# Performance work log

Measured on AMD Instinct MI355X. Metric: run time of the kernel, lower is better.

## Reference

```python
import jax, jax.numpy as jnp
import numpy as np


def leaky(x):
    return jnp.where(x > 0, x, 0.2 * x)


def conv(x, w, b, s, p):
    y = jax.lax.conv_general_dilated(x, w, (s, s), [(p, p), (p, p)],
                                     dimension_numbers=('NCHW', 'OIHW', 'NCHW'))
    return y + b[None, :, None, None]


def maxpool2s1(x):
    return jax.lax.reduce_window(x, -jnp.inf, jax.lax.max, (1, 1, 2, 2), (1, 1, 1, 1), 'VALID')


def bn_eval(x, g, b, m, v):
    scale = g / jnp.sqrt(v + 1e-5)
    return (x - m[None, :, None, None]) * scale[None, :, None, None] + b[None, :, None, None]


def adaptive_avg_pool(x, oh, ow):
    # matches torch AdaptiveAvgPool2d window rule: [floor(i*H/o), ceil((i+1)*H/o))
    B, C, H, W = x.shape
    rows = []
    for i in range(oh):
        hs, he = (i * H) // oh, -((-(i + 1) * H) // oh)
        cols = []
        for j in range(ow):
            ws, we = (j * W) // ow, -((-(j + 1) * W) // ow)
            cols.append(x[:, :, hs:he, ws:we].mean((2, 3)))
        rows.append(jnp.stack(cols, -1))
    return jnp.stack(rows, -2)  # [B,C,oh,ow]


def forward(x, tw1, tb1, tw2, tb2, tw3, tb3, tw4, tb4,
            sw1, sb1, bn1_g, bn1_b, bn1_m, bn1_v,
            sw2, sb2, bn2_g, bn2_b, bn2_m, bn2_v,
            cw, cb, ew1, eb1, ew2, eb2, ew3, eb3):
    B = x.shape[0]
    E, K = ew1.shape[0], 2
    # --- scout router (BN in eval mode with running stats) ---
    h = jax.nn.relu(bn_eval(conv(x, sw1, sb1, 4, 3), bn1_g, bn1_b, bn1_m, bn1_v))
    h = jax.nn.relu(bn_eval(conv(h, sw2, sb2, 2, 1), bn2_g, bn2_b, bn2_m, bn2_v))
    logits = h.mean((2, 3)) @ cw.T + cb                       # [B,E]
    gate = jax.nn.softmax(logits, axis=-1)
    topk_p, topk_i = jax.lax.top_k(gate, K)                   # [B,K]
    topk_p = topk_p / (topk_p.sum(-1, keepdims=True) + 1e-6)
    # --- shared trunk ---
    t = maxpool2s1(leaky(conv(x, tw1, tb1, 4, 1)))            # 224->56->55
    t = maxpool2s1(leaky(conv(t, tw2, tb2, 2, 2)))            # 55->28->27
    t = leaky(conv(t, tw3, tb3, 1, 1))                        # 27
    t = maxpool2s1(leaky(conv(t, tw4, tb4, 1, 1)))            # 27->26
    t = adaptive_avg_pool(t, 3, 3)                            # [B,128,3,3]
    flat = t.reshape(B, -1)                                   # [B,1152]
    # --- MoE head: dense per-expert MLP, masked weighted combine ---
    h1 = leaky(jnp.einsum('bi,eoi->beo', flat, ew1) + eb1[None])   # [B,E,1024]
    h2 = leaky(jnp.einsum('beh,eoh->beo', h1, ew2) + eb2[None])    # [B,E,512]
    h3 = jnp.einsum('beh,eoh->beo', h2, ew3) + eb3[None]           # [B,E,feat]
    onehot = (topk_i[:, :, None] == jnp.arange(E)[None, None, :])  # [B,K,E]
    comb_w = jnp.sum(topk_p[:, :, None] * onehot, axis=1)          # [B,E]
    out = jnp.einsum('beo,be->bo', h3, comb_w)                     # [B,feat]
    return out


def setup_inputs() -> dict:
    key = jax.random.key(0)
    ks = jax.random.split(key, 32)
    W = 0.02
    d = {}
    d['x'] = jax.random.normal(ks[0], (256, 3, 224, 224), jnp.float32)
    d['tw1'] = jax.random.normal(ks[1], (16, 3, 3, 3), jnp.float32) * W
    d['tb1'] = jnp.zeros((16,), jnp.float32)
    d['tw2'] = jax.random.normal(ks[2], (32, 16, 5, 5), jnp.float32) * W
    d['tb2'] = jnp.zeros((32,), jnp.float32)
    d['tw3'] = jax.random.normal(ks[3], (64, 32, 3, 3), jnp.float32) * W
    d['tb3'] = jnp.zeros((64,), jnp.float32)
    d['tw4'] = jax.random.normal(ks[4], (128, 64, 3, 3), jnp.float32) * W
    d['tb4'] = jnp.zeros((128,), jnp.float32)
    d['sw1'] = jax.random.normal(ks[5], (16, 3, 7, 7), jnp.float32) * W
    d['sb1'] = jnp.zeros((16,), jnp.float32)
    d['bn1_g'] = jnp.ones((16,), jnp.float32)
    d['bn1_b'] = jnp.zeros((16,), jnp.float32)
    d['bn1_m'] = jnp.zeros((16,), jnp.float32)
    d['bn1_v'] = jnp.ones((16,), jnp.float32)
    d['sw2'] = jax.random.normal(ks[6], (32, 16, 3, 3), jnp.float32) * W
    d['sb2'] = jnp.zeros((32,), jnp.float32)
    d['bn2_g'] = jnp.ones((32,), jnp.float32)
    d['bn2_b'] = jnp.zeros((32,), jnp.float32)
    d['bn2_m'] = jnp.zeros((32,), jnp.float32)
    d['bn2_v'] = jnp.ones((32,), jnp.float32)
    d['cw'] = jax.random.normal(ks[7], (3, 32), jnp.float32) * W
    d['cb'] = jnp.zeros((3,), jnp.float32)
    d['ew1'] = jax.random.normal(ks[8], (3, 1024, 1152), jnp.float32) * W
    d['eb1'] = jnp.zeros((3, 1024), jnp.float32)
    d['ew2'] = jax.random.normal(ks[9], (3, 512, 1024), jnp.float32) * W
    d['eb2'] = jnp.zeros((3, 512), jnp.float32)
    d['ew3'] = jax.random.normal(ks[10], (3, 512, 512), jnp.float32) * W
    d['eb3'] = jnp.zeros((3, 512), jnp.float32)
    return d


def reference(x, tw1, tb1, tw2, tb2, tw3, tb3, tw4, tb4,
              sw1, sb1, bn1_g, bn1_b, bn1_m, bn1_v,
              sw2, sb2, bn2_g, bn2_b, bn2_m, bn2_v,
              cw, cb, ew1, eb1, ew2, eb2, ew3, eb3):
    return forward(x, tw1, tb1, tw2, tb2, tw3, tb3, tw4, tb4,
                   sw1, sb1, bn1_g, bn1_b, bn1_m, bn1_v,
                   sw2, sb2, bn2_g, bn2_b, bn2_m, bn2_v,
                   cw, cb, ew1, eb1, ew2, eb2, ew3, eb3)
```

## Files before the change

### kernel.cpp

```cpp
#include <hip/hip_runtime.h>

#define DEV static __device__ __forceinline__

constexpr int BATCH = 256;

DEV float leakyf(float x){ return x > 0.f ? x : 0.2f * x; }

typedef _Float16 f16x8 __attribute__((ext_vector_type(8)));
typedef float f32x4 __attribute__((ext_vector_type(4)));

DEV f16x8 max8(f16x8 a, f16x8 b){
  f16x8 r;
  #pragma unroll
  for (int j = 0; j < 8; ++j) r[j] = a[j] > b[j] ? a[j] : b[j];
  return r;
}

template<int IC,int OC>
DEV void wpackM_body(int i, const float* __restrict__ w, _Float16* __restrict__ wp){
  constexpr int F = OC/16;
  int j = i & 7, L = (i >> 3) & 63, rest = i >> 9;
  int f = rest % F; int q2 = rest / F; int s = q2 % (IC/32); int t = q2 / (IC/32);
  int oc = f*16 + (L & 15), ic = s*32 + (L >> 4)*8 + j;
  wp[i] = (_Float16)w[((size_t)oc*IC + ic)*9 + t];
}

template<int OC,int K>
DEV void wpackS_body(int i, const float* __restrict__ w, _Float16* __restrict__ wp){
  constexpr int F = OC/16, KWP = (K+1)/2;
  int j = i & 7, L = (i >> 3) & 63, rest = i >> 9;
  int f = rest % F, s = rest / F;
  int kh = s / KWP, kwp = s % KWP;
  int k = (L >> 4)*8 + j;
  int kw = 2*kwp + (k >> 4), ic = k & 15;
  int oc = f*16 + (L & 15);
  float v = (kw < K) ? w[((size_t)(oc*16 + ic)*K + kh)*K + kw] : 0.f;
  wp[i] = (_Float16)v;
}

DEV void wpackF_body(int i, const float* __restrict__ sw1,
                     const float* __restrict__ tw1, _Float16* __restrict__ wp){
  int j = i & 7, L = (i >> 3) & 63, rest = i >> 9;
  int nf = rest & 1, s = rest >> 1;
  int k = s*32 + (L >> 4)*8 + j;
  int oc = L & 15;
  int t = k / 48, c = k % 48;
  int dr = (t >> 1) - 1, dc = (t & 1) - 1;
  int ic = c >> 4, pr = (c >> 2) & 3, pc = c & 3;
  float v = 0.f;
  if (nf == 0){
    int kh = 4*dr + pr + 3, kw = 4*dc + pc + 3;
    if (kh >= 0 && kh < 7 && kw >= 0 && kw < 7) v = sw1[((oc*3 + ic)*7 + kh)*7 + kw];
  } else {
    int kh = 4*dr + pr + 1, kw = 4*dc + pc + 1;
    if (kh >= 0 && kh < 3 && kw >= 0 && kw < 3) v = tw1[((oc*3 + ic)*3 + kh)*3 + kw];
  }
  wp[i] = (_Float16)v;
}

template<int KTOT>
DEV void wpackG_body(int i, int e, const float* __restrict__ w, int N,
                     _Float16* __restrict__ wp){
  const int NF = N >> 4;
  const int total = NF * (KTOT >> 5) * 512;
  w  += (size_t)e * N * KTOT;
  wp += (size_t)e * total;
  int j = i & 7, L = (i >> 3) & 63, rest = i >> 9;
  int nf = rest % NF, t = rest / NF;
  int n = nf*16 + (L & 15), k = t*32 + (L >> 4)*8 + j;
  wp[i] = (_Float16)w[(size_t)n*KTOT + k];
}

__global__ __launch_bounds__(256) void wpackX_k(
    const float* __restrict__ tw3, _Float16* __restrict__ wpk3,
    const float* __restrict__ tw4, _Float16* __restrict__ wpk4,
    const float* __restrict__ tw2, _Float16* __restrict__ wp2,
    const float* __restrict__ sw2, _Float16* __restrict__ wps2,
    const float* __restrict__ sw1, const float* __restrict__ tw1,
    _Float16* __restrict__ wpf,
    const float* __restrict__ ew1, _Float16* __restrict__ ewp1,
    const float* __restrict__ ew2, _Float16* __restrict__ ewp2,
    const float* __restrict__ ew3, _Float16* __restrict__ ewp3){
  const int b = blockIdx.x;
  const int tid = threadIdx.x;
  if (b < 72){
    wpackM_body<32,64>(b*256 + tid, tw3, wpk3);
  } else if (b < 360){
    wpackM_body<64,128>((b-72)*256 + tid, tw4, wpk4);
  } else if (b < 420){
    wpackS_body<32,5>((b-360)*256 + tid, tw2, wp2);
  } else if (b < 444){
    wpackS_body<32,3>((b-420)*256 + tid, sw2, wps2);
  } else if (b < 468){
    wpackF_body((b-444)*256 + tid, sw1, tw1, wpf);
  } else {
    int t = b - 468;
    if (t < 13824){
      wpackG_body<1152>((t % 4608)*256 + tid, t / 4608, ew1, 1024, ewp1);
    } else if (t < 19968){
      int t2 = t - 13824;
      wpackG_body<1024>((t2 % 2048)*256 + tid, t2 / 2048, ew2, 512, ewp2);
    } else {
      int t3 = t - 19968;
      wpackG_body<512>((t3 % 1024)*256 + tid, t3 / 1024, ew3, 512, ewp3);
    }
  }
}

__global__ __launch_bounds__(256) void fusedM_k(
    const float* __restrict__ x,
    const _Float16* __restrict__ W,
    const float* __restrict__ sb, const float* __restrict__ cb_,
    const float* __restrict__ g, const float* __restrict__ bt,
    const float* __restrict__ mn, const float* __restrict__ vr,
    _Float16* __restrict__ s1out, _Float16* __restrict__ c1out){
  __shared__ __align__(16) _Float16 Ah[3*58*64];
  const int tid = threadIdx.x;
  const int n = blockIdx.x / 28, oh0 = (blockIdx.x % 28) * 2;

  if (tid < 48){
    int rr = tid >> 4, side = (tid >> 3) & 1, q = tid & 7;
    int col = side ? 57 : 0;
    *(int4*)((char*)Ah + (((rr*58 + col) << 7) + q*16)) = (int4){0,0,0,0};
  }

  {
    const int m = tid & 63;
    const bool mok = (m < 56);
    const int cc = m + 1;
    int rc0 = tid >> 6;
    int ic   = (rc0 == 3) ? 0 : rc0;
    int ridx = (rc0 == 3) ? 1 : 0;
    #pragma unroll
    for (int j = 0; j < 9; ++j){
      const int ih = 4*oh0 - 4 + ridx;
      if (mok){
        float4 v = {0.f,0.f,0.f,0.f};
        if (ih >= 0)
          v = *(const float4*)(x + ((size_t)(n*3 + ic)*224 + ih)*224 + 4*m);
        const int rr = ridx >> 2, pr = ridx & 3;
        int boff = (((rr*58 + cc) << 7) + ic*32 + pr*8) ^ ((cc & 7) << 4);
        _Float16 h4[4] = {(_Float16)v.x, (_Float16)v.y, (_Float16)v.z, (_Float16)v.w};
        *(unsigned long long*)((char*)Ah + boff) = *(unsigned long long*)h4;
      }
      ic += 1; ridx += 1;
      if (ic >= 3){ ic -= 3; ridx += 1; }
    }
  }
  __syncthreads();

  const int wid = tid >> 6, lane = tid & 63;
  const int kg8 = (lane >> 4) * 8;
  f32x4 acc[2][2];
  #pragma unroll
  for (int mi = 0; mi < 2; ++mi)
    #pragma unroll
    for (int nf = 0; nf < 2; ++nf) acc[mi][nf] = (f32x4){0.f,0.f,0.f,0.f};

  #pragma unroll
  for (int s = 0; s < 6; ++s){
    const int kk = s*32 + kg8;
    const int t = kk / 48, c0 = kk - t*48;
    const int ra = t >> 1, ca = t & 1;
    f16x8 ah[2];
    #pragma unroll
    for (int mi = 0; mi < 2; ++mi){
      const int m = 2*wid + mi;
      const int rowsel = m >> 2;
      const int ow = (m & 3)*16 + (lane & 15);
      const int owc = ow > 55 ? 55 : ow;
      const int col = owc + ca;
      const int bidx = ((((rowsel + ra)*58 + col) << 7) + c0*2) ^ ((col & 7) << 4);
      ah[mi] = *(const f16x8*)((const char*)Ah + bidx);
    }
    #pragma unroll
    for (int nf = 0; nf < 2; ++nf){
      const f16x8 bw = *(const f16x8*)(W + (s*2 + nf)*512 + lane*8);
      #pragma unroll
      for (int mi = 0; mi < 2; ++mi)
        acc[mi][nf] = __builtin_amdgcn_mfma_f32_16x16x32_f16(ah[mi], bw, acc[mi][nf], 0,0,0);
    }
  }

  const int oc = lane & 15;
  const float sbv = sb[oc];
  const float scv = g[oc] * __frsqrt_rn(vr[oc] + 1e-5f);
  const float mnv = mn[oc], btv = bt[oc], cbv = cb_[oc];
  #pragma unroll
  for (int mi = 0; mi < 2; ++mi){
    const int m = 2*wid + mi;
    const int row = oh0 + (m >> 2);
    const int owb = (m & 3)*16 + (lane >> 4)*4;
    #pragma unroll
    for (int r = 0; r < 4; ++r){
      const int ow = owb + r;
      if (ow >= 56) continue;
      float vs = acc[mi][0][r] + sbv;
      vs = fmaxf((vs - mnv)*scv + btv, 0.f);
      const size_t o = (((size_t)n*56 + row)*56 + ow)*16 + oc;
      s1out[o] = (_Float16)vs;
      c1out[o] = (_Float16)leakyf(acc[mi][1][r] + cbv);
    }
  }
}

template<int OC,int K,int P,int IH,int IW,int ACT,bool OUT16,bool GATE,bool POOLIN>
DEV void convS_body(int bx, int tid, _Float16* A, float* gred,
    const _Float16* __restrict__ in,
    const _Float16* __restrict__ W,
    const float* __restrict__ bias,
    const float* __restrict__ bng, const float* __restrict__ bnb,
    const float* __restrict__ bnm, const float* __restrict__ bnv,
    float* __restrict__ outF, _Float16* __restrict__ outH,
    float* __restrict__ gsum){
  constexpr int F = OC/16, KWP = (K+1)/2;
  constexpr int RW = POOLIN ? (IW+1) : IW;

  const int n = bx / 28, oh = bx % 28;

  if (GATE && tid < 32) gred[tid] = 0.f;

  for (int i = tid; i < K*60*2; i += 256){
    int half = i & 1; int p = i >> 1;
    int c = p % 60; int r = p / 60;
    int ih = 2*oh - P + r, iw = c - P;
    int4 v = {0,0,0,0};
    if (ih >= 0 && ih < IH && iw >= 0 && iw < IW){
      const _Float16* q = in + (((size_t)n*(POOLIN ? IH+1 : IH) + ih)*RW + iw)*16 + half*8;
      if (POOLIN){
        f16x8 a = *(const f16x8*)q;
        f16x8 b = *(const f16x8*)(q + 16);
        f16x8 cc = *(const f16x8*)(q + RW*16);
        f16x8 d = *(const f16x8*)(q + RW*16 + 16);
        f16x8 mx = max8(max8(a, b), max8(cc, d));
        v = *(int4*)&mx;
      } else {
        v = *(const int4*)q;
      }
    }
    int byte = ((r*60 + c)*32 + half*16) ^ (((c>>1)&7) << 4);
    *(int4*)((char*)A + byte) = v;
  }
  __syncthreads();

  const int wid = tid >> 6, lane = tid & 63;
  const int fsel = wid & 1, mb = wid >> 1;
  const int ow_l = min(mb*16 + (lane & 15), 27);
  const int ic0b = ((lane >> 4) & 1) * 16;
  const int kwo  = (lane >> 4) >> 1;

  f32x4 acc = {0.f,0.f,0.f,0.f};
  #pragma unroll
  for (int kh = 0; kh < K; ++kh){
    #pragma unroll
    for (int kwp = 0; kwp < KWP; ++kwp){
      const int kw = 2*kwp + kwo;
      const int c = 2*ow_l + kw;
      int byte = ((kh*60 + c)*32 + ic0b) ^ (((c>>1)&7) << 4);
      f16x8 a = *(const f16x8*)((const char*)A + byte);
      const int s = kh*KWP + kwp;
      const f16x8 b = *(const f16x8*)(W + (s*F + fsel)*512 + lane*8);
      acc = __builtin_amdgcn_mfma_f32_16x16x32_f16(a, b, acc, 0,0,0);
    }
  }

  const int oc = fsel*16 + (lane & 15);
  float bv = bias[oc], sc = 1.f, mm = 0.f, bb = 0.f;
  if (ACT == 1){
    sc = bng[oc] * __frsqrt_rn(bnv[oc] + 1e-5f);
    mm = bnm[oc]; bb = bnb[oc];
  }
  float lsum = 0.f;
  #pragma unroll
  for (int r = 0; r < 4; ++r){
    const int ow = mb*16 + (lane >> 4)*4 + r;
    if (ow >= 28) continue;
    float v = acc[r] + bv;
    if (ACT == 1) v = fmaxf((v - mm)*sc + bb, 0.f);
    else          v = leakyf(v);
    if (GATE){
      lsum += v;
    } else {
      const size_t o = (((size_t)n*28 + oh)*28 + ow)*OC + oc;
      if (OUT16) outH[o] = (_Float16)v;
      else       outF[o] = v;
    }
  }
  if (GATE){
    atomicAdd(&gred[oc], lsum);
    __syncthreads();
    if (tid < 32) atomicAdd(&gsum[n*32 + tid], gred[tid]);
  }
}

__global__ __launch_bounds__(256) void convSS_k(
    const _Float16* __restrict__ s1h, const _Float16* __restrict__ wps2,
    const float* __restrict__ sb2,
    const float* __restrict__ bn2g, const float* __restrict__ bn2b,
    const float* __restrict__ bn2m, const float* __restrict__ bn2v,
    float* __restrict__ gsum,
    const _Float16* __restrict__ c1h, const _Float16* __restrict__ wp2,
    const float* __restrict__ tb2, _Float16* __restrict__ c2h){
  __shared__ __align__(16) _Float16 A[5*60*16];
  __shared__ float gred[32];
  const int tid = threadIdx.x;
  if (blockIdx.x < BATCH*28){
    convS_body<32,3,1,56,56,1,false,true,false>(blockIdx.x, tid, A, gred,
        s1h, wps2, sb2, bn2g, bn2b, bn2m, bn2v, nullptr, nullptr, gsum);
  } else {
    convS_body<32,5,2,55,55,0,true,false,true>(blockIdx.x - BATCH*28, tid, A, gred,
        c1h, wp2, tb2, nullptr, nullptr, nullptr, nullptr, nullptr, c2h, nullptr);
  }
}

template<int IC,int OC,bool POOLIN>
__global__ __launch_bounds__(256) void convM_k(
    const _Float16* __restrict__ Ag,
    const _Float16* __restrict__ W,
    const float* __restrict__ bias,
    _Float16* __restrict__ Out)
{
  constexpr int S = IC/32, FTOT = OC/16, FW = FTOT/2;
  constexpr int ICB = IC*2, ICG = ICB/16;
  __shared__ __align__(16) char A[4*34*ICB];

  const int tid = threadIdx.x;
  const int bx = blockIdx.x;
  const int n = bx / 14, pr = bx % 14;
  const int oh0 = pr * 2;

  for (int g = tid; g < 4*34*ICG; g += 256){
    int r = g / (34*ICG);
    int rem = g - r*(34*ICG);
    int c = rem / ICG, q = rem - c*ICG;
    int ir = oh0 + r - 1, icol = c - 1;
    int4 v = {0,0,0,0};
    if (ir >= 0 && ir < 27 && icol >= 0 && icol < 27){
      if (POOLIN){
        const _Float16* p0 = Ag + (((size_t)n*28 + ir)*28 + icol)*IC + q*8;
        f16x8 a = *(const f16x8*)p0;
        f16x8 b = *(const f16x8*)(p0 + IC);
        f16x8 cc = *(const f16x8*)(p0 + 28*IC);
        f16x8 d = *(const f16x8*)(p0 + 28*IC + IC);
        f16x8 mx = max8(max8(a, b), max8(cc, d));
        v = *(int4*)&mx;
      } else {
        v = *(const int4*)(Ag + (((size_t)n*27 + ir)*27 + icol)*IC + q*8);
      }
    }
    int off = (r*34 + c)*ICB + q*16;
    int swz = off ^ ((c & 7) << 4);
    *(int4*)(A + swz) = v;
  }
  __syncthreads();

  const int wid = tid >> 6, lane = tid & 63;
  const int rsel = wid & 1, ocq = wid >> 1;
  const int c0 = lane & 15, kg = (lane >> 4) * 16;
  const int colb0 = c0*ICB + kg, colb1 = (16 + c0)*ICB + kg;
  int msk[3];
  #pragma unroll
  for (int kw = 0; kw < 3; ++kw) msk[kw] = ((c0 + kw) & 7) << 4;

  f32x4 acc[2][FW];
  #pragma unroll
  for (int m = 0; m < 2; ++m)
    #pragma unroll
    for (int f = 0; f < FW; ++f) acc[m][f] = (f32x4){0.f,0.f,0.f,0.f};

  #pragma unroll
  for (int kh = 0; kh < 3; ++kh){
    #pragma unroll
    for (int kw = 0; kw < 3; ++kw){
      #pragma unroll
      for (int s = 0; s < S; ++s){
        const int fr0 = (((kh*3 + kw)*S + s)*FTOT + ocq*FW) * 512 + lane*8;
        f16x8 b[FW];
        #pragma unroll
        for (int f = 0; f < FW; ++f)
          b[f] = *(const f16x8*)(W + fr0 + f*512);
        const int base = ((rsel + kh)*34 + kw)*ICB + s*64;
        const int o0 = (base + colb0) ^ msk[kw];
        const int o1 = (base + colb1) ^ msk[kw];
        f16x8 a0 = *(const f16x8*)(A + o0);
        f16x8 a1 = *(const f16x8*)(A + o1);
        #pragma unroll
        for (int f = 0; f < FW; ++f){
          acc[0][f] = __builtin_amdgcn_mfma_f32_16x16x32_f16(a0, b[f], acc[0][f], 0,0,0);
          acc[1][f] = __builtin_amdgcn_mfma_f32_16x16x32_f16(a1, b[f], acc[1][f], 0,0,0);
        }
      }
    }
  }

  const int orow = oh0 + rsel;
  if (orow >= 27) return;
  #pragma unroll
  for (int f = 0; f < FW; ++f){
    const int oc = (ocq*FW + f)*16 + c0;
    const float bv = bias[oc];
    #pragma unroll
    for (int m = 0; m < 2; ++m){
      #pragma unroll
      for (int r = 0; r < 4; ++r){
        const int ow = m*16 + (lane >> 4)*4 + r;
        if (ow >= 27) continue;
        float v = leakyf(acc[m][f][r] + bv);
        Out[(((size_t)n*27 + orow)*27 + ow)*OC + oc] = (_Float16)v;
      }
    }
  }
}

template<int KTOT,int ACT>
__global__ __launch_bounds__(256) void gemmH_k(
    const _Float16* __restrict__ A, long strideA,
    const _Float16* __restrict__ W,
    const float* __restrict__ bias, int N,
    _Float16* __restrict__ OutH){
  const int e = blockIdx.z;
  A += (size_t)e * strideA;
  const int NF = N >> 4, KT = KTOT >> 5;
  W += (size_t)e * NF * KT * 512;
  const float* bs = bias + (size_t)e * N;
  const size_t ob = (size_t)e * 256 * N;

  const int tid = threadIdx.x, wid = tid >> 6, lane = tid & 63;
  const int mblk = blockIdx.x * 32;
  const int nf = blockIdx.y * 4 + wid;
  const int r0 = mblk + (lane & 15);
  const int kof = (lane >> 4) * 8;

  f32x4 acc0 = {0,0,0,0}, acc1 = {0,0,0,0};
  for (int t = 0; t < KT; ++t){
    const int k = t*32 + kof;
    f16x8 a0 = *(const f16x8*)(A + (size_t)r0*KTOT + k);
    f16x8 a1 = *(const f16x8*)(A + (size_t)(r0+16)*KTOT + k);
    const f16x8 b = *(const f16x8*)(W + ((size_t)t*NF + nf)*512 + lane*8);
    acc0 = __builtin_amdgcn_mfma_f32_16x16x32_f16(a0, b, acc0, 0,0,0);
    acc1 = __builtin_amdgcn_mfma_f32_16x16x32_f16(a1, b, acc1, 0,0,0);
  }
  const int n = nf*16 + (lane & 15);
  const float bv = bs[n];
  #pragma unroll
  for (int mi = 0; mi < 2; ++mi){
    f32x4 a = mi ? acc1 : acc0;
    #pragma unroll
    for (int r = 0; r < 4; ++r){
      const int m = mblk + mi*16 + (lane >> 4)*4 + r;
      float v = a[r] + bv;
      if (ACT == 1) v = leakyf(v);
      OutH[ob + (size_t)m*N + n] = (_Float16)v;
    }
  }
}

__global__ __launch_bounds__(256) void gemmC_k(
    const _Float16* __restrict__ A,
    const _Float16* __restrict__ W,
    const float* __restrict__ b3,
    const float* __restrict__ gsum,
    const float* __restrict__ cw, const float* __restrict__ cb,
    float* __restrict__ out){
  __shared__ float combL[16][3];
  const int tid = threadIdx.x, wid = tid >> 6, lane = tid & 63;
  const int mblk = blockIdx.x * 16;

  if (tid < 16){
    const int n = mblk + tid;
    float mch[32];
    #pragma unroll
    for (int c = 0; c < 32; ++c) mch[c] = gsum[n*32 + c] / 784.f;
    float lg[3];
    #pragma unroll
    for (int e = 0; e < 3; ++e){
      float a = cb[e];
      #pragma unroll
      for (int c = 0; c < 32; ++c) a += mch[c] * cw[e*32 + c];
      lg[e] = a;
    }
    float m = fmaxf(lg[0], fmaxf(lg[1], lg[2]));
    float ex[3], sum = 0.f;
    #pragma unroll
    for (int e = 0; e < 3; ++e){ ex[e] = expf(lg[e] - m); sum += ex[e]; }
    float pr[3];
    #pragma unroll
    for (int e = 0; e < 3; ++e) pr[e] = ex[e] / sum;
    int i1 = 0;
    if (pr[1] > pr[0]) i1 = 1;
    if (pr[2] > pr[i1]) i1 = 2;
    int i2 = -1;
    for (int e = 0; e < 3; ++e){
      if (e == i1) continue;
      if (i2 < 0 || pr[e] > pr[i2]) i2 = e;
    }
    float s12 = pr[i1] + pr[i2] + 1e-6f;
    float cmb[3] = {0.f, 0.f, 0.f};
    cmb[i1] = pr[i1] / s12;
    cmb[i2] = pr[i2] / s12;
    combL[tid][0] = cmb[0];
    combL[tid][1] = cmb[1];
    combL[tid][2] = cmb[2];
  }
  __syncthreads();

  const int nf = blockIdx.y * 4 + wid;
  const int r0 = mblk + (lane & 15);
  const int kof = (lane >> 4) * 8;
  const int n = nf*16 + (lane & 15);

  f32x4 oacc = {0.f,0.f,0.f,0.f};
  #pragma unroll
  for (int e = 0; e < 3; ++e){
    const _Float16* Ae = A + (size_t)e * 256 * 512;
    const _Float16* We = W + (size_t)e * 32 * 16 * 512;
    f32x4 acc = {0.f,0.f,0.f,0.f};
    for (int t = 0; t < 16; ++t){
      f16x8 a = *(const f16x8*)(Ae + (size_t)r0*512 + t*32 + kof);
      const f16x8 b = *(const f16x8*)(We + ((size_t)t*32 + nf)*512 + lane*8);
      acc = __builtin_amdgcn_mfma_f32_16x16x32_f16(a, b, acc, 0,0,0);
    }
    const float bv = b3[e*512 + n];
    #pragma unroll
    for (int r = 0; r < 4; ++r){
      const int lr = (lane >> 4)*4 + r;
      oacc[r] += combL[lr][e] * (acc[r] + bv);
    }
  }
  #pragma unroll
  for (int r = 0; r < 4; ++r){
    const int m = mblk + (lane >> 4)*4 + r;
    out[(size_t)m*512 + n] = oacc[r];
  }
}

__global__ __launch_bounds__(256) void papool2_k(const _Float16* __restrict__ in,
                                                 _Float16* __restrict__ flat16){
  __shared__ float red[2][128][9];
  const int n = blockIdx.x;
  const int tid = threadIdx.x;
  const int h = tid >> 7, c = tid & 127;
  const _Float16* p = in + (size_t)n * 729 * 128 + c;

  float sum[9];
  #pragma unroll
  for (int j = 0; j < 9; ++j) sum[j] = 0.f;

  float prev[27], cur[27];
  const int r0 = h * 13;
  #pragma unroll
  for (int rr = 0; rr < 14; ++rr){
    const int r = r0 + rr;
    #pragma unroll
    for (int cc = 0; cc < 27; ++cc)
      cur[cc] = (float)p[(size_t)(r*27 + cc) * 128];
    if (rr > 0){
      const int pr = r - 1;
      const bool b0 = (pr < 9), b1 = (pr >= 8) && (pr < 18), b2 = (pr >= 17);
      #pragma unroll
      for (int cc = 0; cc < 26; ++cc){
        float v = fmaxf(fmaxf(prev[cc], prev[cc+1]), fmaxf(cur[cc], cur[cc+1]));
        if (b0){
          if (cc < 9)             sum[0] += v;
          if (cc >= 8 && cc < 18) sum[1] += v;
          if (cc >= 17)           sum[2] += v;
        }
        if (b1){
          if (cc < 9)             sum[3] += v;
          if (cc >= 8 && cc < 18) sum[4] += v;
          if (cc >= 17)           sum[5] += v;
        }
        if (b2){
          if (cc < 9)             sum[6] += v;
          if (cc >= 8 && cc < 18) sum[7] += v;
          if (cc >= 17)           sum[8] += v;
        }
      }
    }
    #pragma unroll
    for (int cc = 0; cc < 27; ++cc) prev[cc] = cur[cc];
  }

  #pragma unroll
  for (int j = 0; j < 9; ++j) red[h][c][j] = sum[j];
  __syncthreads();

  if (tid < 128){
    const float rcp[9] = {1.f/81, 1.f/90, 1.f/81, 1.f/90, 1.f/100, 1.f/90,
                          1.f/81, 1.f/90, 1.f/81};
    _Float16* o = flat16 + (size_t)n * 1152 + tid * 9;
    #pragma unroll
    for (int j = 0; j < 9; ++j)
      o[j] = (_Float16)((red[0][tid][j] + red[1][tid][j]) * rcp[j]);
  }
}

extern "C" void kernel_launch(void* const* d_in, const int* in_sizes, int n_in,
                              void* d_out, int out_size, void* d_ws, size_t ws_size,
                              hipStream_t stream){
  const float* x    = (const float*)d_in[0];
  const float* tw1  = (const float*)d_in[1];  const float* tb1 = (const float*)d_in[2];
  const float* tw2  = (const float*)d_in[3];  const float* tb2 = (const float*)d_in[4];
  const float* tw3  = (const float*)d_in[5];  const float* tb3 = (const float*)d_in[6];
  const float* tw4  = (const float*)d_in[7];  const float* tb4 = (const float*)d_in[8];
  const float* sw1  = (const float*)d_in[9];  const float* sb1 = (const float*)d_in[10];
  const float* bn1g = (const float*)d_in[11]; const float* bn1b = (const float*)d_in[12];
  const float* bn1m = (const float*)d_in[13]; const float* bn1v = (const float*)d_in[14];
  const float* sw2  = (const float*)d_in[15]; const float* sb2 = (const float*)d_in[16];
  const float* bn2g = (const float*)d_in[17]; const float* bn2b = (const float*)d_in[18];
  const float* bn2m = (const float*)d_in[19]; const float* bn2v = (const float*)d_in[20];
  const float* cw   = (const float*)d_in[21]; const float* cb  = (const float*)d_in[22];
  const float* ew1  = (const float*)d_in[23]; const float* eb1 = (const float*)d_in[24];
  const float* ew2  = (const float*)d_in[25]; const float* eb2 = (const float*)d_in[26];
  const float* ew3  = (const float*)d_in[27]; const float* eb3 = (const float*)d_in[28];
  float* out = (float*)d_out;

  float* ws = (float*)d_ws;
  size_t off = 0;
  _Float16* flat16 = (_Float16*)(ws + off); off += 147456;
  float* gsum   = ws + off; off += BATCH * 32;
  _Float16* wpk3 = (_Float16*)(ws + off); off += 9216;
  _Float16* wpk4 = (_Float16*)(ws + off); off += 36864;
  _Float16* wp2  = (_Float16*)(ws + off); off += 7680;
  _Float16* wps2 = (_Float16*)(ws + off); off += 3072;
  _Float16* wpf  = (_Float16*)(ws + off); off += 3072;
  off += 16;
  float* bufA   = ws + off; off += 13778944;
  off += 16;
  float* bufB   = ws + off; off += 23887872;
  off += 16;
  (void)ws_size; (void)in_sizes; (void)n_in; (void)out_size;

  _Float16* s1h = (_Float16*)bufA;
  _Float16* C3u = (_Float16*)bufA;
  _Float16* ewp1 = (_Float16*)(bufA + 6500000);
  _Float16* ewp2 = ewp1 + 3538944;
  _Float16* ewp3 = ewp2 + 1572864;
  _Float16* c1h = (_Float16*)bufB;
  _Float16* c2h = (_Float16*)(bufB + 14000000);
  _Float16* c4h = (_Float16*)bufB;
  _Float16* h1  = (_Float16*)bufB;
  _Float16* h2  = h1 + 786432;

  dim3 blk(256);

  hipMemsetAsync(gsum, 0, BATCH * 32 * sizeof(float), stream);
  wpackX_k<<<dim3(23508), blk, 0, stream>>>(
      tw3, wpk3, tw4, wpk4, tw2, wp2, sw2, wps2, sw1, tw1, wpf,
      ew1, ewp1, ew2, ewp2, ew3, ewp3);

  fusedM_k<<<dim3(BATCH*28), blk, 0, stream>>>(
      x, wpf, sb1, tb1, bn1g, bn1b, bn1m, bn1v, s1h, c1h);

  convSS_k<<<dim3(BATCH*28*2), blk, 0, stream>>>(
      s1h, wps2, sb2, bn2g, bn2b, bn2m, bn2v, gsum,
      c1h, wp2, tb2, c2h);

  convM_k<32,64,true><<<dim3(BATCH*14), blk, 0, stream>>>(
      c2h, wpk3, tb3, C3u);

  convM_k<64,128,false><<<dim3(BATCH*14), blk, 0, stream>>>(
      C3u, wpk4, tb4, c4h);

  papool2_k<<<dim3(BATCH), blk, 0, stream>>>(c4h, flat16);

  gemmH_k<1152,1><<<dim3(8,16,3), blk, 0, stream>>>(
      flat16, 0L, ewp1, eb1, 1024, h1);
  gemmH_k<1024,1><<<dim3(8,8,3), blk, 0, stream>>>(
      h1, 256L*1024, ewp2, eb2, 512, h2);
  gemmC_k<<<dim3(16,8), blk, 0, stream>>>(
      h2, ewp3, eb3, gsum, cw, cb, out);
}
```

Baseline: 257.1 us.

## Overlap expert weight packing with first conv and fold memset into pack kernel

Expert GEMM weight packing moves out of the small-weight pack kernel and into the first fused conv kernel as extra leading blocks, so the memory-bound conversion can overlap with the conv work. The gsum zeroing replaces the separate hipMemsetAsync and runs inside the conv-weight pack kernel, removing one launch. The conv block index is also swizzled in groups of eight, which changes block-to-CU placement. The trade-off is a larger fused kernel: its occupancy is set by the conv path's shared memory and registers, and the packing blocks are scheduled ahead of the conv blocks.

```diff
diff --git a/kernel.cpp b/kernel.cpp
--- a/kernel.cpp
+++ b/kernel.cpp
@@ -71,16 +71,13 @@
   wp[i] = (_Float16)w[(size_t)n*KTOT + k];
 }
 
-__global__ __launch_bounds__(256) void wpackX_k(
+__global__ __launch_bounds__(256) void wpackC_k(
     const float* __restrict__ tw3, _Float16* __restrict__ wpk3,
     const float* __restrict__ tw4, _Float16* __restrict__ wpk4,
     const float* __restrict__ tw2, _Float16* __restrict__ wp2,
     const float* __restrict__ sw2, _Float16* __restrict__ wps2,
     const float* __restrict__ sw1, const float* __restrict__ tw1,
-    _Float16* __restrict__ wpf,
-    const float* __restrict__ ew1, _Float16* __restrict__ ewp1,
-    const float* __restrict__ ew2, _Float16* __restrict__ ewp2,
-    const float* __restrict__ ew3, _Float16* __restrict__ ewp3){
+    _Float16* __restrict__ wpf, float* __restrict__ gsum){
   const int b = blockIdx.x;
   const int tid = threadIdx.x;
   if (b < 72){
@@ -94,29 +91,40 @@
   } else if (b < 468){
     wpackF_body((b-444)*256 + tid, sw1, tw1, wpf);
   } else {
-    int t = b - 468;
-    if (t < 13824){
-      wpackG_body<1152>((t % 4608)*256 + tid, t / 4608, ew1, 1024, ewp1);
-    } else if (t < 19968){
-      int t2 = t - 13824;
-      wpackG_body<1024>((t2 % 2048)*256 + tid, t2 / 2048, ew2, 512, ewp2);
-    } else {
-      int t3 = t - 19968;
-      wpackG_body<512>((t3 % 1024)*256 + tid, t3 / 1024, ew3, 512, ewp3);
-    }
-  }
-}
-
-__global__ __launch_bounds__(256) void fusedM_k(
+    gsum[(b-468)*256 + tid] = 0.f;
+  }
+}
+
+__global__ __launch_bounds__(256) void fusedX_k(
     const float* __restrict__ x,
     const _Float16* __restrict__ W,
     const float* __restrict__ sb, const float* __restrict__ cb_,
     const float* __restrict__ g, const float* __restrict__ bt,
     const float* __restrict__ mn, const float* __restrict__ vr,
-    _Float16* __restrict__ s1out, _Float16* __restrict__ c1out){
+    _Float16* __restrict__ s1out, _Float16* __restrict__ c1out,
+    const float* __restrict__ ew1, _Float16* __restrict__ ewp1,
+    const float* __restrict__ ew2, _Float16* __restrict__ ewp2,
+    const float* __restrict__ ew3, _Float16* __restrict__ ewp3){
   __shared__ __align__(16) _Float16 Ah[3*58*64];
   const int tid = threadIdx.x;
-  const int n = blockIdx.x / 28, oh0 = (blockIdx.x % 28) * 2;
+  const int b = blockIdx.x;
+
+  if (b < 23040){
+    if (b < 13824){
+      wpackG_body<1152>((b % 4608)*256 + tid, b / 4608, ew1, 1024, ewp1);
+    } else if (b < 19968){
+      int t2 = b - 13824;
+      wpackG_body<1024>((t2 % 2048)*256 + tid, t2 / 2048, ew2, 512, ewp2);
+    } else {
+      int t3 = b - 19968;
+      wpackG_body<512>((t3 % 1024)*256 + tid, t3 / 1024, ew3, 512, ewp3);
+    }
+    return;
+  }
+
+  const int lb = b - 23040;
+  const int w = (lb & 7)*896 + (lb >> 3);
+  const int n = w / 28, oh0 = (w % 28) * 2;
 
   if (tid < 48){
     int rr = tid >> 4, side = (tid >> 3) & 1, q = tid & 7;
@@ -644,13 +652,12 @@
 
   dim3 blk(256);
 
-  hipMemsetAsync(gsum, 0, BATCH * 32 * sizeof(float), stream);
-  wpackX_k<<<dim3(23508), blk, 0, stream>>>(
-      tw3, wpk3, tw4, wpk4, tw2, wp2, sw2, wps2, sw1, tw1, wpf,
+  wpackC_k<<<dim3(500), blk, 0, stream>>>(
+      tw3, wpk3, tw4, wpk4, tw2, wp2, sw2, wps2, sw1, tw1, wpf, gsum);
+
+  fusedX_k<<<dim3(30208), blk, 0, stream>>>(
+      x, wpf, sb1, tb1, bn1g, bn1b, bn1m, bn1v, s1h, c1h,
       ew1, ewp1, ew2, ewp2, ew3, ewp3);
-
-  fusedM_k<<<dim3(BATCH*28), blk, 0, stream>>>(
-      x, wpf, sb1, tb1, bn1g, bn1b, bn1m, bn1v, s1h, c1h);
 
   convSS_k<<<dim3(BATCH*28*2), blk, 0, stream>>>(
       s1h, wps2, sb2, bn2g, bn2b, bn2m, bn2v, gsum,
```

New measurement: 246.9 us. 1.04x faster.
